# Kernel tuning notes

Measured on AMD Instinct MI355X. Metric: run time of the kernel, lower is better.

## Reference

```python
import jax, jax.numpy as jnp
import numpy as np

B, S, D, H = 2, 2048, 1024, 16
HD = D // H  # head_dim = 64


def setup_inputs() -> dict:
    key = jax.random.key(0)
    k1, k2, k3 = jax.random.split(key, 3)
    x = jax.random.normal(k1, (B, S, D), dtype=jnp.float32)
    W_qkv = jax.random.normal(k2, (D, 3 * D), dtype=jnp.float32) * (D ** -0.5)
    b_qkv = jnp.zeros((3 * D,), dtype=jnp.float32)
    W_proj = jax.random.normal(k3, (D, D), dtype=jnp.float32) * (D ** -0.5)
    b_proj = jnp.zeros((D,), dtype=jnp.float32)
    return {"x": x, "W_qkv": W_qkv, "b_qkv": b_qkv, "W_proj": W_proj, "b_proj": b_proj}


def reference(x, W_qkv, b_qkv, W_proj, b_proj):
    b, s, d = x.shape
    scale = HD ** -0.5
    qkv = x @ W_qkv + b_qkv                       # [B,S,3D]
    q, k, v = jnp.split(qkv, 3, axis=-1)
    # [B,S,D] -> [B,H,S,HD]
    def to_heads(t):
        return t.reshape(b, s, H, HD).transpose(0, 2, 1, 3)
    q, k, v = map(to_heads, (q, k, v))
    scores = jnp.einsum('bhqd,bhkd->bhqk', q, k) * scale  # [B,H,S,S]
    causal = jnp.triu(jnp.ones((s, s), dtype=bool), k=1)
    scores = jnp.where(causal[None, None], -jnp.inf, scores)
    attn = jax.nn.softmax(scores, axis=-1)
    out = jnp.einsum('bhqk,bhkd->bhqd', attn, v)  # [B,H,S,HD]
    out = out.transpose(0, 2, 1, 3).reshape(b, s, d)
    return out @ W_proj + b_proj
```

## Files before the change

kernel.cpp:

```cpp
#include <hip/hip_runtime.h>

using frag_t = __attribute__((ext_vector_type(8))) short;
using f32x4  = __attribute__((ext_vector_type(4))) float;

#define L2E 1.4426950408889634f

constexpr int B_  = 2, S_ = 2048, D_ = 1024, H_ = 16, HD_ = 64;
constexpr int M_  = B_ * S_;
constexpr float QSCALE = 0.125f * L2E;

__device__ __forceinline__ ushort f2bf(float f) {
  union { float f; unsigned u; } v; v.f = f;
  unsigned u = v.u;
  unsigned r = (u + 0x7FFFu + ((u >> 16) & 1u)) >> 16;
  return (ushort)r;
}
__device__ __forceinline__ ushort f2bf_fast(float f) {
  union { float f; unsigned u; } v; v.f = f;
  return (ushort)((v.u + 0x8000u) >> 16);
}

__device__ __forceinline__ void gld_lds16(const ushort* g, ushort* l) {
  __builtin_amdgcn_global_load_lds((const __attribute__((address_space(1))) void*)g,
                                   (__attribute__((address_space(3))) void*)l, 16, 0, 0);
}

__global__ __launch_bounds__(256) void k_prep(
    const float* __restrict__ x, const float* __restrict__ Wqkv,
    const float* __restrict__ Wproj,
    ushort* __restrict__ Xbf, ushort* __restrict__ Wqt, ushort* __restrict__ Wpt) {
  int blk = blockIdx.x, tid = threadIdx.x;
  if (blk < 1024) {
    size_t base = (size_t)blk * 4096 + tid * 4;
    #pragma unroll
    for (int i = 0; i < 4; ++i) {
      float4 f = *(const float4*)(x + base + i * 1024);
      ushort4 o;
      o.x = f2bf(f.x); o.y = f2bf(f.y); o.z = f2bf(f.z); o.w = f2bf(f.w);
      *(ushort4*)(Xbf + base + i * 1024) = o;
    }
  } else {
    __shared__ float tile[64][65];
    const float* in; ushort* out; int N, K, bx, by;
    if (blk < 1024 + 768) { int b2 = blk - 1024; in = Wqkv;  out = Wqt; N = 3072; K = 1024; bx = b2 % 48; by = b2 / 48; }
    else                  { int b2 = blk - 1792; in = Wproj; out = Wpt; N = 1024; K = 1024; bx = b2 % 16; by = b2 / 16; }
    int n0 = bx * 64, k0 = by * 64;
    int tx = tid & 63, ty = tid >> 6;
    #pragma unroll
    for (int i = 0; i < 16; ++i)
      tile[ty + i * 4][tx] = in[(size_t)(k0 + ty + i * 4) * N + n0 + tx];
    __syncthreads();
    #pragma unroll
    for (int i = 0; i < 16; ++i)
      out[(size_t)(n0 + ty + i * 4) * K + k0 + tx] = f2bf(tile[tx][ty + i * 4]);
  }
}

template <int EPI>
__global__ __launch_bounds__(256) void k_gemm(
    const ushort* __restrict__ A, const ushort* __restrict__ Bt,
    const float* __restrict__ bias,
    ushort* __restrict__ Qo, ushort* __restrict__ Ko, ushort* __restrict__ Vo,
    float* __restrict__ Co, int N, int K) {
  constexpr int BM = 128, BN = 128, BK = 64;
  constexpr int SMEM = (EPI == 0) ? 4 * 64 * 72 : (BM + BN) * BK;
  __shared__ ushort smem[SMEM];
  ushort* As = smem;
  ushort* Bs = smem + BM * BK;
  int tid  = threadIdx.x;
  int lane = tid & 63, wave = tid >> 6;
  int quad = lane >> 4, li = lane & 15;
  int wy = wave >> 1, wx = wave & 1;
  int m0 = blockIdx.y * BM, n0 = blockIdx.x * BN;
  int srow = lane >> 3;
  int scol = ((lane & 7) ^ srow) * 8;
  f32x4 acc[4][4] = {};
  for (int k0 = 0; k0 < K; k0 += BK) {
    #pragma unroll
    for (int i = 0; i < 4; ++i) {
      int rbase = i * 32 + wave * 8;
      int r = rbase + srow;
      gld_lds16(&A[(size_t)(m0 + r) * K + k0 + scol], &As[rbase * BK]);
      gld_lds16(&Bt[(size_t)(n0 + r) * K + k0 + scol], &Bs[rbase * BK]);
    }
    __syncthreads();
    #pragma unroll
    for (int ks = 0; ks < 2; ++ks) {
      frag_t af[4], bf[4];
      #pragma unroll
      for (int mi = 0; mi < 4; ++mi)
        af[mi] = *(const frag_t*)&As[(wy * 64 + mi * 16 + li) * BK + (((ks * 4 + quad) ^ (li & 7)) * 8)];
      #pragma unroll
      for (int ni = 0; ni < 4; ++ni)
        bf[ni] = *(const frag_t*)&Bs[(wx * 64 + ni * 16 + li) * BK + (((ks * 4 + quad) ^ (li & 7)) * 8)];
      #pragma unroll
      for (int mi = 0; mi < 4; ++mi)
        #pragma unroll
        for (int ni = 0; ni < 4; ++ni)
          acc[mi][ni] = __builtin_amdgcn_mfma_f32_16x16x32_bf16(af[mi], bf[ni], acc[mi][ni], 0, 0, 0);
    }
    __syncthreads();
  }
  if (EPI == 1) {
    #pragma unroll
    for (int mi = 0; mi < 4; ++mi)
      #pragma unroll
      for (int ni = 0; ni < 4; ++ni) {
        int gcol = n0 + wx * 64 + ni * 16 + li;
        float bv = bias[gcol];
        #pragma unroll
        for (int r = 0; r < 4; ++r) {
          int grow = m0 + wy * 64 + mi * 16 + quad * 4 + r;
          Co[(size_t)grow * N + gcol] = acc[mi][ni][r] + bv;
        }
      }
  } else {
    int which = (n0 + wx * 64) >> 10;
    if (which < 2) {
      #pragma unroll
      for (int mi = 0; mi < 4; ++mi)
        #pragma unroll
        for (int ni = 0; ni < 4; ++ni) {
          int gcol = n0 + wx * 64 + ni * 16 + li;
          float bv = bias[gcol];
          #pragma unroll
          for (int r = 0; r < 4; ++r) {
            int grow = m0 + wy * 64 + mi * 16 + quad * 4 + r;
            float v = acc[mi][ni][r] + bv;
            int d = gcol & 1023, h = d >> 6, hd = d & 63;
            int b = grow >> 11, s = grow & 2047;
            size_t bh = (size_t)b * H_ + h;
            if (which == 0) Qo[(bh * S_ + s) * HD_ + hd] = f2bf(v * QSCALE);
            else            Ko[(bh * S_ + s) * HD_ + hd] = f2bf(v);
          }
        }
    } else {
      ushort* vlds = smem + wave * (64 * 72);
      #pragma unroll
      for (int ni = 0; ni < 4; ++ni) {
        float bv = bias[n0 + wx * 64 + ni * 16 + li];
        #pragma unroll
        for (int mi = 0; mi < 4; ++mi)
          #pragma unroll
          for (int r = 0; r < 4; ++r)
            vlds[(ni * 16 + li) * 72 + mi * 16 + quad * 4 + r] = f2bf(acc[mi][ni][r] + bv);
      }
      int hgrp = ((n0 & 1023) + wx * 64) >> 6;
      int b = m0 >> 11;
      int s0 = (m0 & 2047) + wy * 64;
      size_t vbase = (size_t)(b * H_ + hgrp) * HD_ * S_;
      #pragma unroll
      for (int i = 0; i < 8; ++i) {
        int row = i * 8 + (lane >> 3);
        int col = (lane & 7) * 8;
        *(uint4*)&Vo[vbase + (size_t)row * S_ + s0 + col] = *(const uint4*)&vlds[row * 72 + col];
      }
    }
  }
}

__global__ __launch_bounds__(256) void k_attn(
    const ushort* __restrict__ Q, const ushort* __restrict__ K,
    const ushort* __restrict__ Vt, ushort* __restrict__ O) {
  __shared__ ushort Kbuf[2][64 * 64];
  __shared__ ushort Vbuf[2][64 * 64];
  __shared__ ushort Plds[4 * 16 * 64];
  int lane = threadIdx.x & 63, wave = threadIdx.x >> 6;
  int quad = lane >> 4, li = lane & 15;
  int bh = blockIdx.x;
  int qb = 31 - (int)blockIdx.y;
  int b = bh >> 4, h = bh & 15;
  int q0 = qb * 64 + wave * 16;
  const ushort* Qb = Q  + (size_t)bh * S_ * HD_;
  const ushort* Kb = K  + (size_t)bh * S_ * HD_;
  const ushort* Vb = Vt + (size_t)bh * HD_ * S_;
  ushort* Pw = &Plds[wave * 1024];

  frag_t qf[2];
  #pragma unroll
  for (int ks = 0; ks < 2; ++ks)
    qf[ks] = *(const frag_t*)&Qb[(size_t)(q0 + li) * HD_ + ks * 32 + quad * 8];

  f32x4 o[4] = {};
  float l_r[4] = {0.f, 0.f, 0.f, 0.f};

  auto stage = [&](int kb, int bi) {
    #pragma unroll
    for (int i = 0; i < 2; ++i) {
      int rt  = wave * 16 + i * 8 + (lane >> 3);
      int c16 = (lane & 7) ^ (lane >> 3);
      gld_lds16(&Kb[(size_t)(kb * 64 + rt) * HD_ + c16 * 8], &Kbuf[bi][(wave * 16 + i * 8) * 64]);
      gld_lds16(&Vb[(size_t)rt * S_ + kb * 64 + c16 * 8],    &Vbuf[bi][(wave * 16 + i * 8) * 64]);
    }
  };

  auto comp = [&](int kb, bool diag, int bi) {
    f32x4 sc[4];
    #pragma unroll
    for (int t = 0; t < 4; ++t) {
      f32x4 a = {};
      #pragma unroll
      for (int ks = 0; ks < 2; ++ks) {
        frag_t kf = *(const frag_t*)&Kbuf[bi][(t * 16 + li) * 64 + (((quad + ks * 4) ^ (li & 7)) * 8)];
        a = __builtin_amdgcn_mfma_f32_16x16x32_bf16(qf[ks], kf, a, 0, 0, 0);
      }
      sc[t] = a;
    }
    if (diag) {
      #pragma unroll
      for (int t = 0; t < 4; ++t) {
        int key = kb * 64 + t * 16 + li;
        #pragma unroll
        for (int r = 0; r < 4; ++r)
          if (key > q0 + quad * 4 + r) sc[t][r] = -1e30f;
      }
    }
    #pragma unroll
    for (int t = 0; t < 4; ++t)
      #pragma unroll
      for (int r = 0; r < 4; ++r) {
        float p = exp2f(sc[t][r]);
        l_r[r] += p;
        int row = quad * 4 + r;
        int swr = ((row >> 2) << 1) | (row & 1);
        Pw[row * 64 + (((t * 2 + (li >> 3)) ^ swr) * 8) + (li & 7)] = f2bf_fast(p);
      }
    frag_t pf[2];
    int swl = ((li >> 2) << 1) | (li & 1);
    #pragma unroll
    for (int ks = 0; ks < 2; ++ks)
      pf[ks] = *(const frag_t*)&Pw[li * 64 + (((ks * 4 + quad) ^ swl) * 8)];
    #pragma unroll
    for (int t = 0; t < 4; ++t)
      #pragma unroll
      for (int ks = 0; ks < 2; ++ks) {
        frag_t vf = *(const frag_t*)&Vbuf[bi][(t * 16 + li) * 64 + (((quad + ks * 4) ^ (li & 7)) * 8)];
        o[t] = __builtin_amdgcn_mfma_f32_16x16x32_bf16(pf[ks], vf, o[t], 0, 0, 0);
      }
  };

  stage(0, 0);
  __syncthreads();
  for (int kb = 0; kb <= qb; ++kb) {
    if (kb < qb) stage(kb + 1, (kb + 1) & 1);
    comp(kb, kb == qb, kb & 1);
    __syncthreads();
  }

  #pragma unroll
  for (int r = 0; r < 4; ++r) {
    float t = l_r[r];
    #pragma unroll
    for (int off = 1; off < 16; off <<= 1) t += __shfl_xor(t, off);
    float inv = 1.f / t;
    int srow = q0 + quad * 4 + r;
    #pragma unroll
    for (int ht = 0; ht < 4; ++ht)
      O[((size_t)b * S_ + srow) * D_ + h * 64 + ht * 16 + li] = f2bf(o[ht][r] * inv);
  }
}

extern "C" void kernel_launch(void* const* d_in, const int* in_sizes, int n_in,
                              void* d_out, int out_size, void* d_ws, size_t ws_size,
                              hipStream_t stream) {
  (void)in_sizes; (void)n_in; (void)out_size; (void)ws_size;
  const float* x     = (const float*)d_in[0];
  const float* Wqkv  = (const float*)d_in[1];
  const float* bqkv  = (const float*)d_in[2];
  const float* Wproj = (const float*)d_in[3];
  const float* bproj = (const float*)d_in[4];
  float* out = (float*)d_out;

  char* ws = (char*)d_ws;
  ushort* Xbf = (ushort*)(ws);
  ushort* Wqt = (ushort*)(ws + (8u  << 20));
  ushort* Wpt = (ushort*)(ws + (14u << 20));
  ushort* Qbf = (ushort*)(ws + (16u << 20));
  ushort* Kbf = (ushort*)(ws + (24u << 20));
  ushort* Vtb = (ushort*)(ws + (32u << 20));
  ushort* Obf = Xbf;

  k_prep<<<dim3(2048), dim3(256), 0, stream>>>(x, Wqkv, Wproj, Xbf, Wqt, Wpt);
  k_gemm<0><<<dim3(24, 32), dim3(256), 0, stream>>>(Xbf, Wqt, bqkv, Qbf, Kbf, Vtb,
                                                    (float*)nullptr, 3 * D_, D_);
  k_attn<<<dim3(B_ * H_, 32), dim3(256), 0, stream>>>(Qbf, Kbf, Vtb, Obf);
  k_gemm<1><<<dim3(8, 32), dim3(256), 0, stream>>>(Obf, Wpt, bproj,
                                                   (ushort*)nullptr, (ushort*)nullptr, (ushort*)nullptr,
                                                   out, D_, D_);
}
```

Measured before the change: 190.0 us.

## Triple-buffer GEMM LDS loads and shrink projection GEMM tile

Rewrites the GEMM main loop as a three-stage software pipeline. BK drops to 32, direct global-to-LDS loads are issued two iterations ahead, and a vmcnt wait plus one barrier per iteration replaces the two full syncs per step. The LDS swizzle pattern changes to match the new tile shape. The output projection GEMM moves to 64x128 tiles with a 2x-taller grid to give more blocks on the device. The V-transpose epilogue now reuses the As array as scratch, and that scratch is larger than As, so it relies on As and Bs sitting contiguously in LDS.

```diff
diff --git a/kernel.cpp b/kernel.cpp
--- a/kernel.cpp
+++ b/kernel.cpp
@@ -62,70 +62,93 @@
     const float* __restrict__ bias,
     ushort* __restrict__ Qo, ushort* __restrict__ Ko, ushort* __restrict__ Vo,
     float* __restrict__ Co, int N, int K) {
-  constexpr int BM = 128, BN = 128, BK = 64;
-  constexpr int SMEM = (EPI == 0) ? 4 * 64 * 72 : (BM + BN) * BK;
-  __shared__ ushort smem[SMEM];
-  ushort* As = smem;
-  ushort* Bs = smem + BM * BK;
+  constexpr int BM = (EPI == 0) ? 128 : 64;
+  constexpr int BN = 128, BK = 32;
+  constexpr int MI = 4, NI = (EPI == 0) ? 4 : 2;
+  constexpr int NDMA = (EPI == 0) ? 4 : 3;
+  __shared__ ushort As[3][BM * BK];
+  __shared__ ushort Bs[3][BN * BK];
   int tid  = threadIdx.x;
   int lane = tid & 63, wave = tid >> 6;
   int quad = lane >> 4, li = lane & 15;
-  int wy = wave >> 1, wx = wave & 1;
   int m0 = blockIdx.y * BM, n0 = blockIdx.x * BN;
-  int srow = lane >> 3;
-  int scol = ((lane & 7) ^ srow) * 8;
-  f32x4 acc[4][4] = {};
-  for (int k0 = 0; k0 < K; k0 += BK) {
-    #pragma unroll
-    for (int i = 0; i < 4; ++i) {
-      int rbase = i * 32 + wave * 8;
-      int r = rbase + srow;
-      gld_lds16(&A[(size_t)(m0 + r) * K + k0 + scol], &As[rbase * BK]);
-      gld_lds16(&Bt[(size_t)(n0 + r) * K + k0 + scol], &Bs[rbase * BK]);
-    }
-    __syncthreads();
-    #pragma unroll
-    for (int ks = 0; ks < 2; ++ks) {
-      frag_t af[4], bf[4];
-      #pragma unroll
-      for (int mi = 0; mi < 4; ++mi)
-        af[mi] = *(const frag_t*)&As[(wy * 64 + mi * 16 + li) * BK + (((ks * 4 + quad) ^ (li & 7)) * 8)];
-      #pragma unroll
-      for (int ni = 0; ni < 4; ++ni)
-        bf[ni] = *(const frag_t*)&Bs[(wx * 64 + ni * 16 + li) * BK + (((ks * 4 + quad) ^ (li & 7)) * 8)];
-      #pragma unroll
-      for (int mi = 0; mi < 4; ++mi)
-        #pragma unroll
-        for (int ni = 0; ni < 4; ++ni)
-          acc[mi][ni] = __builtin_amdgcn_mfma_f32_16x16x32_bf16(af[mi], bf[ni], acc[mi][ni], 0, 0, 0);
-    }
-    __syncthreads();
-  }
+  int srow   = lane >> 2;
+  int gchunk = (lane & 3) ^ (srow & 3) ^ ((lane >> 4) & 3);
+  int rsl    = (li ^ (li >> 2)) & 3;
+  int mbase  = (EPI == 0) ? (wave >> 1) * 64 : 0;
+  int nbase  = (EPI == 0) ? (wave & 1) * 64 : wave * 32;
+  int niter  = K / BK;
+
+  auto stage = [&](int it, int b) {
+    int k0 = it * BK;
+    if (EPI == 0) {
+      #pragma unroll
+      for (int i = 0; i < 2; ++i) {
+        int rbase = wave * 32 + i * 16;
+        gld_lds16(&A [(size_t)(m0 + rbase + srow) * K + k0 + gchunk * 8], &As[b][rbase * BK]);
+        gld_lds16(&Bt[(size_t)(n0 + rbase + srow) * K + k0 + gchunk * 8], &Bs[b][rbase * BK]);
+      }
+    } else {
+      int ra = wave * 16;
+      gld_lds16(&A[(size_t)(m0 + ra + srow) * K + k0 + gchunk * 8], &As[b][ra * BK]);
+      #pragma unroll
+      for (int i = 0; i < 2; ++i) {
+        int rbase = wave * 32 + i * 16;
+        gld_lds16(&Bt[(size_t)(n0 + rbase + srow) * K + k0 + gchunk * 8], &Bs[b][rbase * BK]);
+      }
+    }
+  };
+
+  f32x4 acc[MI][NI] = {};
+  stage(0, 0);
+  stage(1, 1);
+  for (int it = 0; it < niter; ++it) {
+    __builtin_amdgcn_s_waitcnt(0x0F70 | NDMA);
+    __builtin_amdgcn_s_barrier();
+    __builtin_amdgcn_sched_barrier(0);
+    int ipre = (it + 2 < niter) ? it + 2 : niter - 1;
+    stage(ipre, (it + 2) % 3);
+    int b = it % 3;
+    frag_t af[MI], bf[NI];
+    #pragma unroll
+    for (int mi = 0; mi < MI; ++mi)
+      af[mi] = *(const frag_t*)&As[b][(mbase + mi * 16 + li) * BK + ((quad ^ rsl) * 8)];
+    #pragma unroll
+    for (int ni = 0; ni < NI; ++ni)
+      bf[ni] = *(const frag_t*)&Bs[b][(nbase + ni * 16 + li) * BK + ((quad ^ rsl) * 8)];
+    #pragma unroll
+    for (int mi = 0; mi < MI; ++mi)
+      #pragma unroll
+      for (int ni = 0; ni < NI; ++ni)
+        acc[mi][ni] = __builtin_amdgcn_mfma_f32_16x16x32_bf16(af[mi], bf[ni], acc[mi][ni], 0, 0, 0);
+  }
+  __syncthreads();
+
   if (EPI == 1) {
     #pragma unroll
-    for (int mi = 0; mi < 4; ++mi)
-      #pragma unroll
-      for (int ni = 0; ni < 4; ++ni) {
-        int gcol = n0 + wx * 64 + ni * 16 + li;
+    for (int mi = 0; mi < MI; ++mi)
+      #pragma unroll
+      for (int ni = 0; ni < NI; ++ni) {
+        int gcol = n0 + nbase + ni * 16 + li;
         float bv = bias[gcol];
         #pragma unroll
         for (int r = 0; r < 4; ++r) {
-          int grow = m0 + wy * 64 + mi * 16 + quad * 4 + r;
+          int grow = m0 + mbase + mi * 16 + quad * 4 + r;
           Co[(size_t)grow * N + gcol] = acc[mi][ni][r] + bv;
         }
       }
   } else {
-    int which = (n0 + wx * 64) >> 10;
+    int which = (n0 + nbase) >> 10;
     if (which < 2) {
       #pragma unroll
-      for (int mi = 0; mi < 4; ++mi)
+      for (int mi = 0; mi < MI; ++mi)
         #pragma unroll
-        for (int ni = 0; ni < 4; ++ni) {
-          int gcol = n0 + wx * 64 + ni * 16 + li;
+        for (int ni = 0; ni < NI; ++ni) {
+          int gcol = n0 + nbase + ni * 16 + li;
           float bv = bias[gcol];
           #pragma unroll
           for (int r = 0; r < 4; ++r) {
-            int grow = m0 + wy * 64 + mi * 16 + quad * 4 + r;
+            int grow = m0 + mbase + mi * 16 + quad * 4 + r;
             float v = acc[mi][ni][r] + bv;
             int d = gcol & 1023, h = d >> 6, hd = d & 63;
             int b = grow >> 11, s = grow & 2047;
@@ -135,19 +158,19 @@
           }
         }
     } else {
-      ushort* vlds = smem + wave * (64 * 72);
-      #pragma unroll
-      for (int ni = 0; ni < 4; ++ni) {
-        float bv = bias[n0 + wx * 64 + ni * 16 + li];
+      ushort* vlds = ((ushort*)As) + wave * (64 * 72);
+      #pragma unroll
+      for (int ni = 0; ni < NI; ++ni) {
+        float bv = bias[n0 + nbase + ni * 16 + li];
         #pragma unroll
-        for (int mi = 0; mi < 4; ++mi)
+        for (int mi = 0; mi < MI; ++mi)
           #pragma unroll
           for (int r = 0; r < 4; ++r)
             vlds[(ni * 16 + li) * 72 + mi * 16 + quad * 4 + r] = f2bf(acc[mi][ni][r] + bv);
       }
-      int hgrp = ((n0 & 1023) + wx * 64) >> 6;
+      int hgrp = ((n0 & 1023) + nbase) >> 6;
       int b = m0 >> 11;
-      int s0 = (m0 & 2047) + wy * 64;
+      int s0 = (m0 & 2047) + mbase;
       size_t vbase = (size_t)(b * H_ + hgrp) * HD_ * S_;
       #pragma unroll
       for (int i = 0; i < 8; ++i) {
@@ -284,7 +307,7 @@
   k_gemm<0><<<dim3(24, 32), dim3(256), 0, stream>>>(Xbf, Wqt, bqkv, Qbf, Kbf, Vtb,
                                                     (float*)nullptr, 3 * D_, D_);
   k_attn<<<dim3(B_ * H_, 32), dim3(256), 0, stream>>>(Qbf, Kbf, Vtb, Obf);
-  k_gemm<1><<<dim3(8, 32), dim3(256), 0, stream>>>(Obf, Wpt, bproj,
+  k_gemm<1><<<dim3(8, 64), dim3(256), 0, stream>>>(Obf, Wpt, bproj,
                                                    (ushort*)nullptr, (ushort*)nullptr, (ushort*)nullptr,
                                                    out, D_, D_);
 }
```

Measured after the change: 194.7 us. 1.02x slower.
